# Optimization experiments

Measured on AMD Instinct MI355X. Metric: run time of the kernel, lower is better.

The kernel has to match this reference:

```python
import jax, jax.numpy as jnp
import numpy as np

ALPHA = 0.2  # LeakyReLU negative slope
NEG_BIG = -9e15

def setup_inputs() -> dict:
    key = jax.random.key(0)
    k1, k2, k3, k4 = jax.random.split(key, 4)
    N, F_in, F_out = 8192, 512, 64
    inp = jax.random.normal(k1, (N, F_in), dtype=jnp.float32)
    adj = jax.random.randint(k2, (N, N), 0, 2, dtype=jnp.int32)
    W = jax.random.normal(k3, (F_in, F_out), dtype=jnp.float32) * (1.414 / np.sqrt(F_in + F_out))
    a = jax.random.normal(k4, (2 * F_out, 1), dtype=jnp.float32) * 0.1
    return {"input": inp, "adj": adj, "W": W, "a": a}

def reference(input, adj, W, a):
    # h: [N, F_out]
    h = input @ W
    F_out = h.shape[1]
    # Decompose a into a1 (source part) and a2 (target part):
    a1 = a[:F_out, 0]   # [F_out]
    a2 = a[F_out:, 0]   # [F_out]
    s1 = h @ a1         # [N]
    s2 = h @ a2         # [N]
    e = s1[:, None] + s2[None, :]                      # [N, N]
    e = jnp.where(e > 0, e, ALPHA * e)                 # LeakyReLU
    e = jnp.where(adj > 0, e, jnp.float32(NEG_BIG))    # mask non-edges
    attention = jax.nn.softmax(e, axis=1)              # [N, N]
    # dropout with p=0.0 / eval mode -> identity
    h_prime = attention @ h                            # [N, F_out]
    return h_prime
```

## Files before the change

### kernel.cpp

```cpp
#include <hip/hip_runtime.h>
#include <hip/hip_bf16.h>

#define ALPHA 0.2f

constexpr int N    = 8192;
constexpr int FIN  = 512;
constexpr int FOUT = 64;
constexpr int NSPLIT = 32;
constexpr int JCHUNK = N / NSPLIT;
constexpr int NB     = N / 8;
constexpr int LROW   = JCHUNK + 8;

typedef __attribute__((ext_vector_type(8))) short short8;
typedef __attribute__((ext_vector_type(4))) float f32x4;

__global__ __launch_bounds__(256) void k0_pack(const int* __restrict__ adj,
                                               unsigned char* __restrict__ bits)
{
    const int lane = threadIdx.x & 63;
    const int wv   = threadIdx.x >> 6;
    const int g    = blockIdx.x * 4 + wv;
    const int i    = g >> 2;
    const int segb = (g & 3) * 4;
    const int* row = adj + (size_t)i * N;

    int4 va[8];
    #pragma unroll
    for (int u = 0; u < 4; ++u) {
        const int jb = (segb + u) * 512 + lane * 8;
        va[2 * u]     = *(const int4*)(row + jb);
        va[2 * u + 1] = *(const int4*)(row + jb + 4);
    }
    #pragma unroll
    for (int u = 0; u < 4; ++u) {
        const int4 a = va[2 * u], b = va[2 * u + 1];
        unsigned int byte =
            (a.x != 0 ?   1u : 0u) | (a.y != 0 ?   2u : 0u) |
            (a.z != 0 ?   4u : 0u) | (a.w != 0 ?   8u : 0u) |
            (b.x != 0 ?  16u : 0u) | (b.y != 0 ?  32u : 0u) |
            (b.z != 0 ?  64u : 0u) | (b.w != 0 ? 128u : 0u);
        bits[(size_t)i * NB + (segb + u) * 64 + lane] = (unsigned char)byte;
    }
}

__global__ __launch_bounds__(256) void k1_proj(
    const float* __restrict__ input, const float* __restrict__ W,
    const float* __restrict__ a, __hip_bfloat16* __restrict__ hbT,
    float* __restrict__ s1, float* __restrict__ s2)
{
    __shared__ __hip_bfloat16 tile[8][64];
    const int tid  = threadIdx.x;
    const int col  = tid & 63;
    const int g    = tid >> 6;
    const int rbase = blockIdx.x * 8;

    float acc[2] = {0.f, 0.f};
    const float* in0 = input + (size_t)(rbase + g * 2) * FIN;

    for (int k = 0; k < FIN; k += 8) {
        float w[8];
        #pragma unroll
        for (int q = 0; q < 8; ++q) w[q] = W[(k + q) * FOUT + col];
        const float4 x0a = *(const float4*)(in0 + 0 * FIN + k);
        const float4 x0b = *(const float4*)(in0 + 0 * FIN + k + 4);
        const float4 x1a = *(const float4*)(in0 + 1 * FIN + k);
        const float4 x1b = *(const float4*)(in0 + 1 * FIN + k + 4);
        acc[0] = fmaf(x0a.w, w[3], fmaf(x0a.z, w[2], fmaf(x0a.y, w[1], fmaf(x0a.x, w[0], acc[0]))));
        acc[0] = fmaf(x0b.w, w[7], fmaf(x0b.z, w[6], fmaf(x0b.y, w[5], fmaf(x0b.x, w[4], acc[0]))));
        acc[1] = fmaf(x1a.w, w[3], fmaf(x1a.z, w[2], fmaf(x1a.y, w[1], fmaf(x1a.x, w[0], acc[1]))));
        acc[1] = fmaf(x1b.w, w[7], fmaf(x1b.z, w[6], fmaf(x1b.y, w[5], fmaf(x1b.x, w[4], acc[1]))));
    }

    const float a1c = a[col];
    const float a2c = a[FOUT + col];
    #pragma unroll
    for (int q = 0; q < 2; ++q) {
        float r1 = acc[q] * a1c;
        float r2 = acc[q] * a2c;
        #pragma unroll
        for (int off = 32; off >= 1; off >>= 1) {
            r1 += __shfl_xor(r1, off, 64);
            r2 += __shfl_xor(r2, off, 64);
        }
        if (col == 0) {
            s1[rbase + g * 2 + q] = r1;
            s2[rbase + g * 2 + q] = r2;
        }
        tile[g * 2 + q][col] = __float2bfloat16(acc[q]);
    }
    __syncthreads();

    if (tid < 128) {
        const int c = tid >> 1, part = tid & 1;
        unsigned short v[4];
        #pragma unroll
        for (int u = 0; u < 4; ++u) {
            __hip_bfloat16 hv = tile[part * 4 + u][c];
            v[u] = *reinterpret_cast<unsigned short*>(&hv);
        }
        *(ushort4*)((unsigned short*)hbT + (size_t)c * N + rbase + part * 4) =
            make_ushort4(v[0], v[1], v[2], v[3]);
    }
}

__global__ __launch_bounds__(256, 4) void k2_attn(
    const unsigned char* __restrict__ bits,
    const float* __restrict__ s1, const float* __restrict__ s2,
    const unsigned short* __restrict__ hbT,
    float* __restrict__ pAcc, float* __restrict__ pZ)
{
    __shared__ unsigned short Bl[64 * LROW];
    __shared__ unsigned int   Ml[64 * 9];
    __shared__ float          S2l[JCHUNK];

    const int r   = blockIdx.x;
    const int s   = blockIdx.y;
    const int tid = threadIdx.x;
    const int w     = tid >> 6;
    const int lane  = tid & 63;
    const int row16 = lane & 15;
    const int quad  = lane >> 4;
    const int jbeg  = s * JCHUNK;

    #pragma unroll
    for (int rr = 0; rr < 8; ++rr) {
        const int seg = rr * 256 + tid;
        const int f = seg >> 5, o = seg & 31;
        const short8 v = *(const short8*)((const short*)hbT + (size_t)f * N + jbeg + o * 8);
        *(short8*)(&Bl[f * LROW + o * 8]) = v;
    }
    #pragma unroll
    for (int rr = 0; rr < 2; ++rr) {
        const int idx = rr * 256 + tid;
        const int row = idx >> 3, col = idx & 7;
        Ml[row * 9 + col] =
            *(const unsigned int*)(bits + (size_t)(r * 64 + row) * NB + (jbeg >> 3) + col * 4);
    }
    S2l[tid] = s2[jbeg + tid];
    __syncthreads();

    const int iloc = w * 16 + row16;
    const int i    = r * 64 + iloc;
    const float s1i = s1[i];

    f32x4 acc0 = {0.f, 0.f, 0.f, 0.f};
    f32x4 acc1 = {0.f, 0.f, 0.f, 0.f};
    f32x4 acc2 = {0.f, 0.f, 0.f, 0.f};
    f32x4 acc3 = {0.f, 0.f, 0.f, 0.f};
    float zpart = 0.f;

    #pragma unroll
    for (int it = 0; it < JCHUNK / 32; ++it) {
        const int j0rel = it * 32;
        const int jj    = j0rel + quad * 8;

        const unsigned int cM    = Ml[iloc * 9 + it];
        const unsigned int mbyte = (cM >> (8 * quad)) & 0xffu;

        const float4 sA = *(const float4*)(&S2l[jj]);
        const float4 sB = *(const float4*)(&S2l[jj + 4]);

        const short8 b0 = *(const short8*)(&Bl[(row16 +  0) * LROW + jj]);
        const short8 b1 = *(const short8*)(&Bl[(row16 + 16) * LROW + jj]);
        const short8 b2 = *(const short8*)(&Bl[(row16 + 32) * LROW + jj]);
        const short8 b3 = *(const short8*)(&Bl[(row16 + 48) * LROW + jj]);

        float s2v[8];
        s2v[0] = sA.x; s2v[1] = sA.y; s2v[2] = sA.z; s2v[3] = sA.w;
        s2v[4] = sB.x; s2v[5] = sB.y; s2v[6] = sB.z; s2v[7] = sB.w;

        short8 afrag;
        #pragma unroll
        for (int j = 0; j < 8; ++j) {
            float e = s1i + s2v[j];
            e = fmaxf(e, ALPHA * e);
            float pv = __expf(e);
            pv = ((mbyte >> j) & 1u) ? pv : 0.f;
            __hip_bfloat16 hv = __float2bfloat16(pv);
            zpart += __bfloat162float(hv);
            afrag[j] = *reinterpret_cast<short*>(&hv);
        }

        acc0 = __builtin_amdgcn_mfma_f32_16x16x32_bf16(afrag, b0, acc0, 0, 0, 0);
        acc1 = __builtin_amdgcn_mfma_f32_16x16x32_bf16(afrag, b1, acc1, 0, 0, 0);
        acc2 = __builtin_amdgcn_mfma_f32_16x16x32_bf16(afrag, b2, acc2, 0, 0, 0);
        acc3 = __builtin_amdgcn_mfma_f32_16x16x32_bf16(afrag, b3, acc3, 0, 0, 0);
    }

    zpart += __shfl_xor(zpart, 16, 64);
    zpart += __shfl_xor(zpart, 32, 64);
    if (quad == 0) pZ[(size_t)s * N + i] = zpart;

    float* outp = pAcc + ((size_t)s * N + (size_t)r * 64 + w * 16) * FOUT;
    #pragma unroll
    for (int reg = 0; reg < 4; ++reg) {
        const int row = quad * 4 + reg;
        outp[row * FOUT + ( 0 + row16)] = acc0[reg];
        outp[row * FOUT + (16 + row16)] = acc1[reg];
        outp[row * FOUT + (32 + row16)] = acc2[reg];
        outp[row * FOUT + (48 + row16)] = acc3[reg];
    }
}

__global__ __launch_bounds__(256) void k3_combine(
    const float* __restrict__ pAcc, const float* __restrict__ pZ,
    float* __restrict__ out)
{
    const int idx = blockIdx.x * 256 + threadIdx.x;
    const int i = idx >> 6;
    float num = 0.f, den = 0.f;
    #pragma unroll
    for (int s = 0; s < NSPLIT; ++s) {
        num += pAcc[(size_t)s * N * FOUT + idx];
        den += pZ[(size_t)s * N + i];
    }
    out[idx] = num / den;
}

extern "C" void kernel_launch(void* const* d_in, const int* in_sizes, int n_in,
                              void* d_out, int out_size, void* d_ws, size_t ws_size,
                              hipStream_t stream)
{
    const float* input = (const float*)d_in[0];
    const int*   adj   = (const int*)d_in[1];
    const float* W     = (const float*)d_in[2];
    const float* a     = (const float*)d_in[3];
    float* out = (float*)d_out;

    char* ws = (char*)d_ws;
    __hip_bfloat16* hbT = (__hip_bfloat16*)ws;
    float* s1   = (float*)(ws + (size_t)FOUT * N * 2);
    float* s2   = s1 + N;
    float* pZ   = s2 + N;
    float* pAcc = pZ + (size_t)NSPLIT * N;
    unsigned char* bitsP = (unsigned char*)(pAcc + (size_t)NSPLIT * N * FOUT);

    k0_pack<<<8192, 256, 0, stream>>>(adj, bitsP);
    k1_proj<<<N / 8, 256, 0, stream>>>(input, W, a, hbT, s1, s2);

    dim3 g2(N / 64, NSPLIT);
    k2_attn<<<g2, 256, 0, stream>>>(bitsP, s1, s2, (const unsigned short*)hbT, pAcc, pZ);

    k3_combine<<<(N * FOUT) / 256, 256, 0, stream>>>(pAcc, pZ, out);
}
```

Before: 471.0 us.

## Fuse adjacency bitpacking into attention kernel and factor exp of LeakyReLU

```diff
diff --git a/kernel.cpp b/kernel.cpp
--- a/kernel.cpp
+++ b/kernel.cpp
@@ -1,52 +1,21 @@
 #include <hip/hip_runtime.h>
 #include <hip/hip_bf16.h>
-
-#define ALPHA 0.2f
 
 constexpr int N    = 8192;
 constexpr int FIN  = 512;
 constexpr int FOUT = 64;
 constexpr int NSPLIT = 32;
 constexpr int JCHUNK = N / NSPLIT;
-constexpr int NB     = N / 8;
 constexpr int LROW   = JCHUNK + 8;
 
 typedef __attribute__((ext_vector_type(8))) short short8;
 typedef __attribute__((ext_vector_type(4))) float f32x4;
-
-__global__ __launch_bounds__(256) void k0_pack(const int* __restrict__ adj,
-                                               unsigned char* __restrict__ bits)
-{
-    const int lane = threadIdx.x & 63;
-    const int wv   = threadIdx.x >> 6;
-    const int g    = blockIdx.x * 4 + wv;
-    const int i    = g >> 2;
-    const int segb = (g & 3) * 4;
-    const int* row = adj + (size_t)i * N;
-
-    int4 va[8];
-    #pragma unroll
-    for (int u = 0; u < 4; ++u) {
-        const int jb = (segb + u) * 512 + lane * 8;
-        va[2 * u]     = *(const int4*)(row + jb);
-        va[2 * u + 1] = *(const int4*)(row + jb + 4);
-    }
-    #pragma unroll
-    for (int u = 0; u < 4; ++u) {
-        const int4 a = va[2 * u], b = va[2 * u + 1];
-        unsigned int byte =
-            (a.x != 0 ?   1u : 0u) | (a.y != 0 ?   2u : 0u) |
-            (a.z != 0 ?   4u : 0u) | (a.w != 0 ?   8u : 0u) |
-            (b.x != 0 ?  16u : 0u) | (b.y != 0 ?  32u : 0u) |
-            (b.z != 0 ?  64u : 0u) | (b.w != 0 ? 128u : 0u);
-        bits[(size_t)i * NB + (segb + u) * 64 + lane] = (unsigned char)byte;
-    }
-}
 
 __global__ __launch_bounds__(256) void k1_proj(
     const float* __restrict__ input, const float* __restrict__ W,
     const float* __restrict__ a, __hip_bfloat16* __restrict__ hbT,
-    float* __restrict__ s1, float* __restrict__ s2)
+    float* __restrict__ E1, float* __restrict__ F1,
+    float* __restrict__ E2, float* __restrict__ F2)
 {
     __shared__ __hip_bfloat16 tile[8][64];
     const int tid  = threadIdx.x;
@@ -83,8 +52,11 @@
             r2 += __shfl_xor(r2, off, 64);
         }
         if (col == 0) {
-            s1[rbase + g * 2 + q] = r1;
-            s2[rbase + g * 2 + q] = r2;
+            const int i = rbase + g * 2 + q;
+            E1[i] = __expf(r1);
+            F1[i] = __expf(0.2f * r1);
+            E2[i] = __expf(r2);
+            F2[i] = __expf(0.2f * r2);
         }
         tile[g * 2 + q][col] = __float2bfloat16(acc[q]);
     }
@@ -104,14 +76,16 @@
 }
 
 __global__ __launch_bounds__(256, 4) void k2_attn(
-    const unsigned char* __restrict__ bits,
-    const float* __restrict__ s1, const float* __restrict__ s2,
+    const int* __restrict__ adj,
+    const float* __restrict__ E1, const float* __restrict__ F1,
+    const float* __restrict__ E2, const float* __restrict__ F2,
     const unsigned short* __restrict__ hbT,
     float* __restrict__ pAcc, float* __restrict__ pZ)
 {
     __shared__ unsigned short Bl[64 * LROW];
     __shared__ unsigned int   Ml[64 * 9];
-    __shared__ float          S2l[JCHUNK];
+    __shared__ float          E2l[JCHUNK];
+    __shared__ float          F2l[JCHUNK];
 
     const int r   = blockIdx.x;
     const int s   = blockIdx.y;
@@ -129,19 +103,28 @@
         const short8 v = *(const short8*)((const short*)hbT + (size_t)f * N + jbeg + o * 8);
         *(short8*)(&Bl[f * LROW + o * 8]) = v;
     }
-    #pragma unroll
-    for (int rr = 0; rr < 2; ++rr) {
-        const int idx = rr * 256 + tid;
-        const int row = idx >> 3, col = idx & 7;
-        Ml[row * 9 + col] =
-            *(const unsigned int*)(bits + (size_t)(r * 64 + row) * NB + (jbeg >> 3) + col * 4);
-    }
-    S2l[tid] = s2[jbeg + tid];
+    {
+        unsigned char* Mlb = (unsigned char*)Ml;
+        #pragma unroll
+        for (int it = 0; it < 16; ++it) {
+            const int rloc = it * 4 + w;
+            const int4 av = *(const int4*)(adj + (size_t)(r * 64 + rloc) * N + jbeg + lane * 4);
+            unsigned int nib =
+                (av.x != 0 ? 1u : 0u) | (av.y != 0 ? 2u : 0u) |
+                (av.z != 0 ? 4u : 0u) | (av.w != 0 ? 8u : 0u);
+            const unsigned int other = __shfl_xor(nib, 1, 64);
+            if (!(lane & 1))
+                Mlb[rloc * 36 + (lane >> 1)] = (unsigned char)(nib | (other << 4));
+        }
+    }
+    E2l[tid] = E2[jbeg + tid];
+    F2l[tid] = F2[jbeg + tid];
     __syncthreads();
 
     const int iloc = w * 16 + row16;
     const int i    = r * 64 + iloc;
-    const float s1i = s1[i];
+    const float E1i = E1[i];
+    const float F1i = F1[i];
 
     f32x4 acc0 = {0.f, 0.f, 0.f, 0.f};
     f32x4 acc1 = {0.f, 0.f, 0.f, 0.f};
@@ -151,30 +134,31 @@
 
     #pragma unroll
     for (int it = 0; it < JCHUNK / 32; ++it) {
-        const int j0rel = it * 32;
-        const int jj    = j0rel + quad * 8;
-
-        const unsigned int cM    = Ml[iloc * 9 + it];
-        const unsigned int mbyte = (cM >> (8 * quad)) & 0xffu;
-
-        const float4 sA = *(const float4*)(&S2l[jj]);
-        const float4 sB = *(const float4*)(&S2l[jj + 4]);
+        const int jj = it * 32 + quad * 8;
+
+        const unsigned int mword = Ml[iloc * 9 + it];
+        const unsigned int mbyte = (mword >> (8 * quad)) & 0xffu;
+
+        const float4 eA = *(const float4*)(&E2l[jj]);
+        const float4 eB = *(const float4*)(&E2l[jj + 4]);
+        const float4 fA = *(const float4*)(&F2l[jj]);
+        const float4 fB = *(const float4*)(&F2l[jj + 4]);
 
         const short8 b0 = *(const short8*)(&Bl[(row16 +  0) * LROW + jj]);
         const short8 b1 = *(const short8*)(&Bl[(row16 + 16) * LROW + jj]);
         const short8 b2 = *(const short8*)(&Bl[(row16 + 32) * LROW + jj]);
         const short8 b3 = *(const short8*)(&Bl[(row16 + 48) * LROW + jj]);
 
-        float s2v[8];
-        s2v[0] = sA.x; s2v[1] = sA.y; s2v[2] = sA.z; s2v[3] = sA.w;
-        s2v[4] = sB.x; s2v[5] = sB.y; s2v[6] = sB.z; s2v[7] = sB.w;
+        float e2v[8], f2v[8];
+        e2v[0] = eA.x; e2v[1] = eA.y; e2v[2] = eA.z; e2v[3] = eA.w;
+        e2v[4] = eB.x; e2v[5] = eB.y; e2v[6] = eB.z; e2v[7] = eB.w;
+        f2v[0] = fA.x; f2v[1] = fA.y; f2v[2] = fA.z; f2v[3] = fA.w;
+        f2v[4] = fB.x; f2v[5] = fB.y; f2v[6] = fB.z; f2v[7] = fB.w;
 
         short8 afrag;
         #pragma unroll
         for (int j = 0; j < 8; ++j) {
-            float e = s1i + s2v[j];
-            e = fmaxf(e, ALPHA * e);
-            float pv = __expf(e);
+            float pv = fmaxf(E1i * e2v[j], F1i * f2v[j]);
             pv = ((mbyte >> j) & 1u) ? pv : 0.f;
             __hip_bfloat16 hv = __float2bfloat16(pv);
             zpart += __bfloat162float(hv);
@@ -229,17 +213,18 @@
 
     char* ws = (char*)d_ws;
     __hip_bfloat16* hbT = (__hip_bfloat16*)ws;
-    float* s1   = (float*)(ws + (size_t)FOUT * N * 2);
-    float* s2   = s1 + N;
-    float* pZ   = s2 + N;
+    float* E1   = (float*)(ws + (size_t)FOUT * N * 2);
+    float* F1   = E1 + N;
+    float* E2   = F1 + N;
+    float* F2   = E2 + N;
+    float* pZ   = F2 + N;
     float* pAcc = pZ + (size_t)NSPLIT * N;
-    unsigned char* bitsP = (unsigned char*)(pAcc + (size_t)NSPLIT * N * FOUT);
-
-    k0_pack<<<8192, 256, 0, stream>>>(adj, bitsP);
-    k1_proj<<<N / 8, 256, 0, stream>>>(input, W, a, hbT, s1, s2);
+
+    k1_proj<<<N / 8, 256, 0, stream>>>(input, W, a, hbT, E1, F1, E2, F2);
 
     dim3 g2(N / 64, NSPLIT);
-    k2_attn<<<g2, 256, 0, stream>>>(bitsP, s1, s2, (const unsigned short*)hbT, pAcc, pZ);
+    k2_attn<<<g2, 256, 0, stream>>>(adj, E1, F1, E2, F2,
+                                    (const unsigned short*)hbT, pAcc, pZ);
 
     k3_combine<<<(N * FOUT) / 256, 256, 0, stream>>>(pAcc, pZ, out);
 }
```

Result: faster. 451.9 us (-4.1%).
